# Performance work log

Hardware: AMD Instinct MI355X
Metric: run time of the kernel (lower is better)

## Reference

```python
import jax, jax.numpy as jnp
import numpy as np

NUM_HEADS = 16

def _split_heads(x, H):
    B, S, D = x.shape
    return x.reshape(B, S, H, D // H).transpose(0, 2, 1, 3)  # [B,H,S,hd]

def _merge_heads(x):
    B, H, S, hd = x.shape
    return x.transpose(0, 2, 1, 3).reshape(B, S, H * hd)

def setup_inputs() -> dict:
    key = jax.random.key(0)
    k1, k2, k3, k4 = jax.random.split(key, 4)
    B, S, D = 2, 2048, 1024
    return {
        "visual_features": jax.random.normal(k1, (B, S, D), dtype=jnp.float32),
        "transaction_features": jax.random.normal(k2, (B, S, D), dtype=jnp.float32),
        "W_qkv": jax.random.normal(k3, (D, 3 * D), dtype=jnp.float32) * (1.0 / np.sqrt(D)),
        "W_out": jax.random.normal(k4, (D, D), dtype=jnp.float32) * (1.0 / np.sqrt(D)),
    }

def reference(visual_features, transaction_features, W_qkv, W_out):
    H = NUM_HEADS
    D = visual_features.shape[-1]
    scale = (D // H) ** -0.5

    v_q, v_k, v_v = [_split_heads(t, H) for t in jnp.split(visual_features @ W_qkv, 3, axis=-1)]
    t_q, t_k, t_v = [_split_heads(t, H) for t in jnp.split(transaction_features @ W_qkv, 3, axis=-1)]

    # visual queries attend to transaction keys/values (dropout = identity at eval)
    v2t = jax.nn.softmax(jnp.einsum('bhqd,bhkd->bhqk', v_q, t_k) * scale, axis=-1)
    t2v = jax.nn.softmax(jnp.einsum('bhqd,bhkd->bhqk', t_q, v_k) * scale, axis=-1)

    v2t_out = _merge_heads(jnp.einsum('bhqk,bhkd->bhqd', v2t, t_v))
    t2v_out = _merge_heads(jnp.einsum('bhqk,bhkd->bhqd', t2v, v_v))

    return (v2t_out + t2v_out) @ W_out
```

## Files before the change

kernel.cpp:

```cpp
#include <hip/hip_runtime.h>


typedef short  frag8 __attribute__((ext_vector_type(8)));
typedef float  f32x4 __attribute__((ext_vector_type(4)));

union F8 { frag8 f; uint2 u2[2]; unsigned u[4]; };

#define MFMA16(a,b,c) __builtin_amdgcn_mfma_f32_16x16x32_bf16((a),(b),(c),0,0,0)

__device__ __forceinline__ unsigned short f2bf(float f) {
  unsigned u = __builtin_bit_cast(unsigned, f);
  return (unsigned short)((u + 0x7fffu + ((u >> 16) & 1u)) >> 16);
}
__device__ __forceinline__ float bf2f(unsigned short s) {
  unsigned u = ((unsigned)s) << 16;
  return __builtin_bit_cast(float, u);
}
__device__ __forceinline__ unsigned pkbf(float lo, float hi) {
  unsigned r;
  asm("v_cvt_pk_bf16_f32 %0, %1, %2" : "=v"(r) : "v"(lo), "v"(hi));
  return r;
}
__device__ __forceinline__ float fexp2(float x) {
  float r;
  asm("v_exp_f32 %0, %1" : "=v"(r) : "v"(x));
  return r;
}

__global__ __launch_bounds__(256) void k_pre(
    const float* __restrict__ vis, const float* __restrict__ trn,
    const float* __restrict__ Wqkv, const float* __restrict__ Wout,
    unsigned short* __restrict__ Abf, unsigned short* __restrict__ WqbT,
    unsigned short* __restrict__ WobT)
{
  __shared__ unsigned short L[64 * 72];
  const int bid = blockIdx.x;
  const int tid = threadIdx.x;

  if (bid < 4096) {
    size_t i8 = ((size_t)bid * 256 + tid) * 8;
    const float* src = (i8 < 4194304) ? vis + i8 : trn + (i8 - 4194304);
    float4 u = *(const float4*)src;
    float4 v = *(const float4*)(src + 4);
    uint4 w;
    w.x = pkbf(u.x, u.y); w.y = pkbf(u.z, u.w);
    w.z = pkbf(v.x, v.y); w.w = pkbf(v.z, v.w);
    *(uint4*)(Abf + i8) = w;
    return;
  }

  const float* W; unsigned short* Wt; int N, bx, by;
  if (bid < 4864) { int b = bid - 4096; W = Wqkv; Wt = WqbT; N = 3072; bx = b % 48; by = b / 48; }
  else            { int b = bid - 4864; W = Wout; Wt = WobT; N = 1024; bx = b % 16; by = b / 16; }
  const int n0 = bx * 64, k0 = by * 64;
  {
    int kr = tid >> 2, c4 = (tid & 3) * 16;
    const float* gp = W + (size_t)(k0 + kr) * N + n0 + c4;
    float4 u0 = *(const float4*)gp,       u1 = *(const float4*)(gp + 4);
    float4 u2 = *(const float4*)(gp + 8), u3 = *(const float4*)(gp + 12);
    unsigned* lw = (unsigned*)&L[kr * 72 + c4];
    lw[0] = pkbf(u0.x, u0.y); lw[1] = pkbf(u0.z, u0.w);
    lw[2] = pkbf(u1.x, u1.y); lw[3] = pkbf(u1.z, u1.w);
    lw[4] = pkbf(u2.x, u2.y); lw[5] = pkbf(u2.z, u2.w);
    lw[6] = pkbf(u3.x, u3.y); lw[7] = pkbf(u3.z, u3.w);
  }
  __syncthreads();
  int nr = tid >> 2, kc = (tid & 3) * 16;
  unsigned wb[8];
#pragma unroll
  for (int j = 0; j < 8; ++j) {
    unsigned lo = L[(kc + 2 * j)     * 72 + nr];
    unsigned hi = L[(kc + 2 * j + 1) * 72 + nr];
    wb[j] = lo | (hi << 16);
  }
  unsigned short* op = Wt + (size_t)(n0 + nr) * 1024 + k0 + kc;
  *(uint4*)op       = *(uint4*)&wb[0];
  *(uint4*)(op + 8) = *(uint4*)&wb[4];
}

__global__ __launch_bounds__(256) void k_gemm_qkv_b(
    const unsigned short* __restrict__ Abf, const unsigned short* __restrict__ WqbT,
    unsigned short* __restrict__ qkv)
{
  __shared__ unsigned short As_[128 * 32];
  __shared__ unsigned short Bs_[128 * 32];
  const int tid  = threadIdx.x;
  const int lane = tid & 63, wv = tid >> 6;
  const int lm = lane & 15, lg = lane >> 4;
  const int wg = (blockIdx.x & 7) * 192 + (blockIdx.x >> 3);
  const int nt = wg % 24, mt = wg / 24;
  const int wr = (wv >> 1) * 64, wc = (wv & 1) * 64;

  f32x4 acc[4][4] = {};

  const unsigned short* agp =
      Abf + (size_t)(mt * 128 + wv * 32 + (lane >> 2)) * 1024 + (lane & 3) * 8;
  const unsigned short* bgp =
      WqbT + (size_t)(nt * 128 + wv * 32 + (lane >> 2)) * 1024 + (lane & 3) * 8;

  for (int kt = 0; kt < 32; ++kt) {
    __syncthreads();
    __builtin_amdgcn_global_load_lds(
        (const __attribute__((address_space(1))) void*)(agp + kt * 32),
        (__attribute__((address_space(3))) void*)&As_[wv * 1024], 16, 0, 0);
    __builtin_amdgcn_global_load_lds(
        (const __attribute__((address_space(1))) void*)(agp + 16 * 1024 + kt * 32),
        (__attribute__((address_space(3))) void*)&As_[wv * 1024 + 512], 16, 0, 0);
    __builtin_amdgcn_global_load_lds(
        (const __attribute__((address_space(1))) void*)(bgp + kt * 32),
        (__attribute__((address_space(3))) void*)&Bs_[wv * 1024], 16, 0, 0);
    __builtin_amdgcn_global_load_lds(
        (const __attribute__((address_space(1))) void*)(bgp + 16 * 1024 + kt * 32),
        (__attribute__((address_space(3))) void*)&Bs_[wv * 1024 + 512], 16, 0, 0);
    __syncthreads();
    frag8 af[4], bfr[4];
#pragma unroll
    for (int mi = 0; mi < 4; ++mi)
      af[mi] = *(const frag8*)&As_[(wr + mi * 16 + lm) * 32 + lg * 8];
#pragma unroll
    for (int ni = 0; ni < 4; ++ni)
      bfr[ni] = *(const frag8*)&Bs_[(wc + ni * 16 + lm) * 32 + lg * 8];
#pragma unroll
    for (int mi = 0; mi < 4; ++mi)
#pragma unroll
      for (int ni = 0; ni < 4; ++ni)
        acc[mi][ni] = MFMA16(af[mi], bfr[ni], acc[mi][ni]);
  }

#pragma unroll
  for (int mi = 0; mi < 4; ++mi)
#pragma unroll
    for (int ni = 0; ni < 4; ++ni)
#pragma unroll
      for (int r = 0; r < 4; ++r) {
        int row = mt * 128 + wr + mi * 16 + lg * 4 + r;
        int col = nt * 128 + wc + ni * 16 + lm;
        qkv[(size_t)row * 3072 + col] = f2bf(acc[mi][ni][r]);
      }
}

__global__ __launch_bounds__(256) void k_vt(
    const unsigned short* __restrict__ qkv, unsigned short* __restrict__ Vt)
{
  __shared__ unsigned short L[64 * 72];
  const int tid = threadIdx.x;
  const int sblk = blockIdx.x;
  const int by = blockIdx.y;
  const int src = by >> 4, h = by & 15;
  {
    int sl = tid >> 2, dc = tid & 3;
    const unsigned short* gp =
        qkv + (size_t)(src * 2048 + sblk * 64 + sl) * 3072 + 2048 + h * 64 + dc * 16;
    *(frag8*)&L[sl * 72 + dc * 16]     = *(const frag8*)gp;
    *(frag8*)&L[sl * 72 + dc * 16 + 8] = *(const frag8*)(gp + 8);
  }
  __syncthreads();
  int d = tid >> 2, sc = tid & 3;
  unsigned wbuf[8];
#pragma unroll
  for (int j = 0; j < 8; ++j) {
    unsigned lo = L[(sc * 16 + 2 * j)     * 72 + d];
    unsigned hi = L[(sc * 16 + 2 * j + 1) * 72 + d];
    wbuf[j] = lo | (hi << 16);
  }
  unsigned short* op =
      Vt + ((size_t)(src * 16 + h) * 64 + d) * 2048 + sblk * 64 + sc * 16;
  *(uint4*)op       = *(uint4*)&wbuf[0];
  *(uint4*)(op + 8) = *(uint4*)&wbuf[4];
}

__global__ __launch_bounds__(256) void k_attn(
    const unsigned short* __restrict__ qkv, const unsigned short* __restrict__ Vt,
    unsigned short* __restrict__ Opart, float* __restrict__ lpart)
{
  __shared__ unsigned short Ks[2][32 * 72];
  __shared__ unsigned short Vs[2][8 * 272];
  const int tid  = threadIdx.x;
  const int lane = tid & 63, wv = tid >> 6;
  const int lm = lane & 15, lg = lane >> 4;
  const int qt = blockIdx.x, comb = blockIdx.y;
  const int dir = comb >> 5, bb = (comb >> 4) & 1, h = comb & 15;
  const int half = blockIdx.z;
  const int NT = 32, kt0 = half * 32;
  const int qbase  = (dir ? 4096 : 0) + bb * 2048;
  const int kvbase = (dir ? 0 : 4096) + bb * 2048;
  const int qcol = h * 64, kcol = 1024 + h * 64;

  const float QS = 0.125f * 1.44269504f;
  frag8 qf[2][2];
#pragma unroll
  for (int mi = 0; mi < 2; ++mi)
#pragma unroll
    for (int kb = 0; kb < 2; ++kb) {
      frag8 t = *(const frag8*)&qkv[
          (size_t)(qbase + qt * 128 + wv * 32 + mi * 16 + lm) * 3072 +
          qcol + kb * 32 + lg * 8];
#pragma unroll
      for (int j = 0; j < 8; ++j)
        t[j] = (short)f2bf(bf2f((unsigned short)t[j]) * QS);
      qf[mi][kb] = t;
    }

  f32x4 acc[2][4] = {};
  float lr[2] = {0.0f, 0.0f};

  const int skv = tid >> 3, sd = (tid & 7) * 8;
  const int vd = tid >> 2, vc = tid & 3;
  const unsigned short* __restrict__ kpp =
      qkv + (size_t)(kvbase + kt0 * 32 + skv) * 3072 + kcol + sd;
  const unsigned short* __restrict__ vpp =
      Vt + ((size_t)((kvbase >> 11) * 16 + h) * 64 + vd) * 2048 + kt0 * 32 + vc * 8;

  frag8 Rk, Rv;

#define LOAD_R() do {                                                      \
    Rk = *(const frag8*)kpp;  kpp += 32 * 3072;                            \
    Rv = *(const frag8*)vpp;  vpp += 32;                                   \
  } while (0)

#define WRITE_R(s_) do {                                                   \
    *(frag8*)&Ks[s_][skv * 72 + sd] = Rk;                                  \
    F8 tv_; tv_.f = Rv;                                                    \
    *(uint2*)&Vs[s_][(2 * vc) * 272 + vd * 4]     = tv_.u2[0];             \
    *(uint2*)&Vs[s_][(2 * vc + 1) * 272 + vd * 4] = tv_.u2[1];             \
  } while (0)

  LOAD_R();
  WRITE_R(0);
  LOAD_R();

  for (int i = 0; i < NT; ++i) {
    __syncthreads();
    if (i < NT - 1) WRITE_R((i + 1) & 1);
    if (i < NT - 2) LOAD_R();
    const int s = i & 1;

    frag8 kf[2][2];
#pragma unroll
    for (int t = 0; t < 2; ++t)
#pragma unroll
      for (int kb = 0; kb < 2; ++kb)
        kf[t][kb] = *(const frag8*)&Ks[s][(t * 16 + lm) * 72 + kb * 32 + lg * 8];
    f32x4 st[2][2] = {};
#pragma unroll
    for (int mi = 0; mi < 2; ++mi)
#pragma unroll
      for (int t = 0; t < 2; ++t)
#pragma unroll
        for (int kb = 0; kb < 2; ++kb)
          st[mi][t] = MFMA16(kf[t][kb], qf[mi][kb], st[mi][t]);

    frag8 pa[2];
#pragma unroll
    for (int mi = 0; mi < 2; ++mi) {
      f32x4 a = st[mi][0], b = st[mi][1];
      float p[8];
#pragma unroll
      for (int r = 0; r < 4; ++r) p[r]     = fexp2(a[r]);
#pragma unroll
      for (int r = 0; r < 4; ++r) p[4 + r] = fexp2(b[r]);
      lr[mi] += ((p[0] + p[1]) + (p[2] + p[3])) +
                ((p[4] + p[5]) + (p[6] + p[7]));
      F8 pk_;
      pk_.u[0] = pkbf(p[0], p[1]); pk_.u[1] = pkbf(p[2], p[3]);
      pk_.u[2] = pkbf(p[4], p[5]); pk_.u[3] = pkbf(p[6], p[7]);
      pa[mi] = pk_.f;
    }

    frag8 vb[4];
#pragma unroll
    for (int di = 0; di < 4; ++di) {
      F8 t;
      t.u2[0] = *(const uint2*)&Vs[s][lg * 272 + (di * 16 + lm) * 4];
      t.u2[1] = *(const uint2*)&Vs[s][(4 + lg) * 272 + (di * 16 + lm) * 4];
      vb[di] = t.f;
    }
#pragma unroll
    for (int mi = 0; mi < 2; ++mi)
#pragma unroll
      for (int di = 0; di < 4; ++di)
        acc[mi][di] = MFMA16(pa[mi], vb[di], acc[mi][di]);
  }

#undef LOAD_R
#undef WRITE_R

#pragma unroll
  for (int mi = 0; mi < 2; ++mi) {
    float l = lr[mi];
    l += __shfl_xor(l, 16);
    l += __shfl_xor(l, 32);
    int rowb = bb * 2048 + qt * 128 + wv * 32 + mi * 16;
    if (lane < 16)
      lpart[(size_t)(half * 2 + dir) * 65536 + h * 4096 + rowb + lane] = l;
#pragma unroll
    for (int r = 0; r < 4; ++r) {
      int row = rowb + lg * 4 + r;
#pragma unroll
      for (int di = 0; di < 4; ++di) {
        int col = h * 64 + di * 16 + lm;
        Opart[((size_t)(half * 2 + dir) * 4096 + row) * 1024 + col] =
            f2bf(acc[mi][di][r]);
      }
    }
  }
}

__global__ __launch_bounds__(256) void k_gemm_out_b(
    const unsigned short* __restrict__ Op, const float* __restrict__ lp,
    const unsigned short* __restrict__ WobT, float* __restrict__ out)
{
  __shared__ unsigned short As[128 * 40];
  __shared__ unsigned short Bs_[128 * 32];
  const int tid  = threadIdx.x;
  const int lane = tid & 63, wv = tid >> 6;
  const int lm = lane & 15, lg = lane >> 4;
  const int wg = (blockIdx.x & 7) * 32 + (blockIdx.x >> 3);
  const int nt = wg % 8, mt = wg / 8;
  const int wr = (wv >> 1) * 64, wc = (wv & 1) * 64;

  f32x4 acc[4][4] = {};

  const int am = tid >> 1, akq = (tid & 1) * 16;
  const int arow = mt * 128 + am;
  const unsigned short* __restrict__ p00 = Op + (size_t)arow * 1024;
  const unsigned short* __restrict__ p01 = p00 + (size_t)4096 * 1024;
  const unsigned short* __restrict__ p10 = p00 + (size_t)2 * 4096 * 1024;
  const unsigned short* __restrict__ p11 = p00 + (size_t)3 * 4096 * 1024;
  const unsigned short* bgp =
      WobT + (size_t)(nt * 128 + wv * 32 + (lane >> 2)) * 1024 + (lane & 3) * 8;

  for (int kt = 0; kt < 32; ++kt) {
    __syncthreads();
    __builtin_amdgcn_global_load_lds(
        (const __attribute__((address_space(1))) void*)(bgp + kt * 32),
        (__attribute__((address_space(3))) void*)&Bs_[wv * 1024], 16, 0, 0);
    __builtin_amdgcn_global_load_lds(
        (const __attribute__((address_space(1))) void*)(bgp + 16 * 1024 + kt * 32),
        (__attribute__((address_space(3))) void*)&Bs_[wv * 1024 + 512], 16, 0, 0);
    {
      const int kcol = kt * 32 + akq;
      const int hh = kt >> 1;
      float inv0 = 1.0f / (lp[hh * 4096 + arow]          + lp[131072 + hh * 4096 + arow]);
      float inv1 = 1.0f / (lp[65536 + hh * 4096 + arow]  + lp[196608 + hh * 4096 + arow]);
      frag8 u0 = *(const frag8*)(p00 + kcol);
      frag8 u1 = *(const frag8*)(p00 + kcol + 8);
      frag8 v0 = *(const frag8*)(p10 + kcol);
      frag8 v1 = *(const frag8*)(p10 + kcol + 8);
      frag8 w0 = *(const frag8*)(p01 + kcol);
      frag8 w1 = *(const frag8*)(p01 + kcol + 8);
      frag8 x0 = *(const frag8*)(p11 + kcol);
      frag8 x1 = *(const frag8*)(p11 + kcol + 8);
      frag8 q0, q1;
#pragma unroll
      for (int j = 0; j < 8; ++j) {
        float a0 = (bf2f((unsigned short)u0[j]) + bf2f((unsigned short)v0[j])) * inv0 +
                   (bf2f((unsigned short)w0[j]) + bf2f((unsigned short)x0[j])) * inv1;
        float a1 = (bf2f((unsigned short)u1[j]) + bf2f((unsigned short)v1[j])) * inv0 +
                   (bf2f((unsigned short)w1[j]) + bf2f((unsigned short)x1[j])) * inv1;
        q0[j] = (short)f2bf(a0);
        q1[j] = (short)f2bf(a1);
      }
      *(frag8*)&As[am * 40 + akq]     = q0;
      *(frag8*)&As[am * 40 + akq + 8] = q1;
    }
    __syncthreads();
    frag8 af[4], bfr[4];
#pragma unroll
    for (int mi = 0; mi < 4; ++mi)
      af[mi] = *(const frag8*)&As[(wr + mi * 16 + lm) * 40 + lg * 8];
#pragma unroll
    for (int ni = 0; ni < 4; ++ni)
      bfr[ni] = *(const frag8*)&Bs_[(wc + ni * 16 + lm) * 32 + lg * 8];
#pragma unroll
    for (int mi = 0; mi < 4; ++mi)
#pragma unroll
      for (int ni = 0; ni < 4; ++ni)
        acc[mi][ni] = MFMA16(af[mi], bfr[ni], acc[mi][ni]);
  }

#pragma unroll
  for (int mi = 0; mi < 4; ++mi)
#pragma unroll
    for (int ni = 0; ni < 4; ++ni)
#pragma unroll
      for (int r = 0; r < 4; ++r) {
        int row = mt * 128 + wr + mi * 16 + lg * 4 + r;
        int col = nt * 128 + wc + ni * 16 + lm;
        out[(size_t)row * 1024 + col] = acc[mi][ni][r];
      }
}

extern "C" void kernel_launch(void* const* d_in, const int* in_sizes, int n_in,
                              void* d_out, int out_size, void* d_ws, size_t ws_size,
                              hipStream_t stream)
{
  const float* vis  = (const float*)d_in[0];
  const float* trn  = (const float*)d_in[1];
  const float* Wqkv = (const float*)d_in[2];
  const float* Wout = (const float*)d_in[3];
  float* out = (float*)d_out;

  char* base = (char*)d_ws;
  unsigned short* qkv  = (unsigned short*)base;
  unsigned short* Vt   = (unsigned short*)(base + 67108864UL);
  unsigned short* WobT = (unsigned short*)(base + 83886080UL);
  float*          lp   = (float*)(base + 85983232UL);
  unsigned short* Abf  = (unsigned short*)(base + 87031808UL);
  unsigned short* WqbT = Abf + 8388608;
  unsigned short* Op   = (unsigned short*)(base + 87031808UL);

  k_pre       <<<5120, 256, 0, stream>>>(vis, trn, Wqkv, Wout, Abf, WqbT, WobT);
  k_gemm_qkv_b<<<1536, 256, 0, stream>>>(Abf, WqbT, qkv);
  k_vt        <<<dim3(32, 64), 256, 0, stream>>>(qkv, Vt);
  k_attn      <<<dim3(16, 64, 2), 256, 0, stream>>>(qkv, Vt, Op, lp);
  k_gemm_out_b<<<256, 256, 0, stream>>>(Op, lp, WobT, out);
}
```

Measured before the change: 236.2 us.

## Drop attention KV split, normalize in attention, process two KV tiles per barrier

The attention kernel no longer splits the 2048 keys into two halves across blockIdx.z. Each block now walks all 64 KV tiles, two tiles per iteration, with a four-stage shared buffer, so it hits the barrier half as often. Softmax normalization moves into the attention epilogue, which writes normalized bf16 outputs for each direction; the output GEMM then just sums two inputs instead of reading four partials plus the row sums. This cuts partial-output traffic and per-element work in the GEMM, but halves the attention grid to 1024 blocks and doubles per-block serial length and LDS use, which may hurt occupancy and load balance.

```diff
diff --git a/kernel.cpp b/kernel.cpp
--- a/kernel.cpp
+++ b/kernel.cpp
@@ -171,17 +171,15 @@
 
 __global__ __launch_bounds__(256) void k_attn(
     const unsigned short* __restrict__ qkv, const unsigned short* __restrict__ Vt,
-    unsigned short* __restrict__ Opart, float* __restrict__ lpart)
-{
-  __shared__ unsigned short Ks[2][32 * 72];
-  __shared__ unsigned short Vs[2][8 * 272];
+    unsigned short* __restrict__ o0, unsigned short* __restrict__ o1)
+{
+  __shared__ unsigned short Ks[4][32 * 72];
+  __shared__ unsigned short Vs[4][8 * 272];
   const int tid  = threadIdx.x;
   const int lane = tid & 63, wv = tid >> 6;
   const int lm = lane & 15, lg = lane >> 4;
   const int qt = blockIdx.x, comb = blockIdx.y;
   const int dir = comb >> 5, bb = (comb >> 4) & 1, h = comb & 15;
-  const int half = blockIdx.z;
-  const int NT = 32, kt0 = half * 32;
   const int qbase  = (dir ? 4096 : 0) + bb * 2048;
   const int kvbase = (dir ? 0 : 4096) + bb * 2048;
   const int qcol = h * 64, kcol = 1024 + h * 64;
@@ -207,107 +205,132 @@
   const int skv = tid >> 3, sd = (tid & 7) * 8;
   const int vd = tid >> 2, vc = tid & 3;
   const unsigned short* __restrict__ kpp =
-      qkv + (size_t)(kvbase + kt0 * 32 + skv) * 3072 + kcol + sd;
+      qkv + (size_t)(kvbase + skv) * 3072 + kcol + sd;
   const unsigned short* __restrict__ vpp =
-      Vt + ((size_t)((kvbase >> 11) * 16 + h) * 64 + vd) * 2048 + kt0 * 32 + vc * 8;
-
-  frag8 Rk, Rv;
-
-#define LOAD_R() do {                                                      \
-    Rk = *(const frag8*)kpp;  kpp += 32 * 3072;                            \
-    Rv = *(const frag8*)vpp;  vpp += 32;                                   \
+      Vt + ((size_t)((kvbase >> 11) * 16 + h) * 64 + vd) * 2048 + vc * 8;
+
+  frag8 R0k, R0v, R1k, R1v;
+
+#define LOAD2() do {                                                       \
+    R0k = *(const frag8*)kpp;  kpp += 32 * 3072;                           \
+    R0v = *(const frag8*)vpp;  vpp += 32;                                  \
+    R1k = *(const frag8*)kpp;  kpp += 32 * 3072;                           \
+    R1v = *(const frag8*)vpp;  vpp += 32;                                  \
   } while (0)
 
-#define WRITE_R(s_) do {                                                   \
-    *(frag8*)&Ks[s_][skv * 72 + sd] = Rk;                                  \
-    F8 tv_; tv_.f = Rv;                                                    \
+#define WRITE1(s_, Rk_, Rv_) do {                                          \
+    *(frag8*)&Ks[s_][skv * 72 + sd] = Rk_;                                 \
+    F8 tv_; tv_.f = Rv_;                                                   \
     *(uint2*)&Vs[s_][(2 * vc) * 272 + vd * 4]     = tv_.u2[0];             \
     *(uint2*)&Vs[s_][(2 * vc + 1) * 272 + vd * 4] = tv_.u2[1];             \
   } while (0)
 
-  LOAD_R();
-  WRITE_R(0);
-  LOAD_R();
-
-  for (int i = 0; i < NT; ++i) {
+  LOAD2();
+  WRITE1(0, R0k, R0v);
+  WRITE1(1, R1k, R1v);
+  LOAD2();
+  __syncthreads();
+
+  for (int j = 0; j < 32; ++j) {
+    const int p = j & 1;
+    if (j < 31) {
+      WRITE1(2 * (p ^ 1),     R0k, R0v);
+      WRITE1(2 * (p ^ 1) + 1, R1k, R1v);
+    }
+    if (j < 30) LOAD2();
+
+    const int sA = 2 * p, sB = 2 * p + 1;
+
+    frag8 kfA[2][2], kfB[2][2];
+#pragma unroll
+    for (int t = 0; t < 2; ++t)
+#pragma unroll
+      for (int kb = 0; kb < 2; ++kb) {
+        kfA[t][kb] = *(const frag8*)&Ks[sA][(t * 16 + lm) * 72 + kb * 32 + lg * 8];
+        kfB[t][kb] = *(const frag8*)&Ks[sB][(t * 16 + lm) * 72 + kb * 32 + lg * 8];
+      }
+    f32x4 stA[2][2] = {}, stB[2][2] = {};
+#pragma unroll
+    for (int mi = 0; mi < 2; ++mi)
+#pragma unroll
+      for (int t = 0; t < 2; ++t)
+#pragma unroll
+        for (int kb = 0; kb < 2; ++kb) {
+          stA[mi][t] = MFMA16(kfA[t][kb], qf[mi][kb], stA[mi][t]);
+          stB[mi][t] = MFMA16(kfB[t][kb], qf[mi][kb], stB[mi][t]);
+        }
+
+    frag8 paA[2], paB[2];
+#pragma unroll
+    for (int mi = 0; mi < 2; ++mi) {
+      f32x4 a = stA[mi][0], b = stA[mi][1];
+      f32x4 c = stB[mi][0], d = stB[mi][1];
+      float p0[8], p1[8];
+#pragma unroll
+      for (int r = 0; r < 4; ++r) {
+        p0[r] = fexp2(a[r]); p0[4 + r] = fexp2(b[r]);
+        p1[r] = fexp2(c[r]); p1[4 + r] = fexp2(d[r]);
+      }
+      lr[mi] += (((p0[0] + p0[1]) + (p0[2] + p0[3])) +
+                 ((p0[4] + p0[5]) + (p0[6] + p0[7]))) +
+                (((p1[0] + p1[1]) + (p1[2] + p1[3])) +
+                 ((p1[4] + p1[5]) + (p1[6] + p1[7])));
+      F8 ka, kb2;
+      ka.u[0]  = pkbf(p0[0], p0[1]); ka.u[1]  = pkbf(p0[2], p0[3]);
+      ka.u[2]  = pkbf(p0[4], p0[5]); ka.u[3]  = pkbf(p0[6], p0[7]);
+      kb2.u[0] = pkbf(p1[0], p1[1]); kb2.u[1] = pkbf(p1[2], p1[3]);
+      kb2.u[2] = pkbf(p1[4], p1[5]); kb2.u[3] = pkbf(p1[6], p1[7]);
+      paA[mi] = ka.f;
+      paB[mi] = kb2.f;
+    }
+
+    frag8 vbA[4], vbB[4];
+#pragma unroll
+    for (int di = 0; di < 4; ++di) {
+      F8 ta, tb;
+      ta.u2[0] = *(const uint2*)&Vs[sA][lg * 272 + (di * 16 + lm) * 4];
+      ta.u2[1] = *(const uint2*)&Vs[sA][(4 + lg) * 272 + (di * 16 + lm) * 4];
+      tb.u2[0] = *(const uint2*)&Vs[sB][lg * 272 + (di * 16 + lm) * 4];
+      tb.u2[1] = *(const uint2*)&Vs[sB][(4 + lg) * 272 + (di * 16 + lm) * 4];
+      vbA[di] = ta.f;
+      vbB[di] = tb.f;
+    }
+#pragma unroll
+    for (int mi = 0; mi < 2; ++mi)
+#pragma unroll
+      for (int di = 0; di < 4; ++di) {
+        acc[mi][di] = MFMA16(paA[mi], vbA[di], acc[mi][di]);
+        acc[mi][di] = MFMA16(paB[mi], vbB[di], acc[mi][di]);
+      }
+
     __syncthreads();
-    if (i < NT - 1) WRITE_R((i + 1) & 1);
-    if (i < NT - 2) LOAD_R();
-    const int s = i & 1;
-
-    frag8 kf[2][2];
-#pragma unroll
-    for (int t = 0; t < 2; ++t)
-#pragma unroll
-      for (int kb = 0; kb < 2; ++kb)
-        kf[t][kb] = *(const frag8*)&Ks[s][(t * 16 + lm) * 72 + kb * 32 + lg * 8];
-    f32x4 st[2][2] = {};
-#pragma unroll
-    for (int mi = 0; mi < 2; ++mi)
-#pragma unroll
-      for (int t = 0; t < 2; ++t)
-#pragma unroll
-        for (int kb = 0; kb < 2; ++kb)
-          st[mi][t] = MFMA16(kf[t][kb], qf[mi][kb], st[mi][t]);
-
-    frag8 pa[2];
-#pragma unroll
-    for (int mi = 0; mi < 2; ++mi) {
-      f32x4 a = st[mi][0], b = st[mi][1];
-      float p[8];
-#pragma unroll
-      for (int r = 0; r < 4; ++r) p[r]     = fexp2(a[r]);
-#pragma unroll
-      for (int r = 0; r < 4; ++r) p[4 + r] = fexp2(b[r]);
-      lr[mi] += ((p[0] + p[1]) + (p[2] + p[3])) +
-                ((p[4] + p[5]) + (p[6] + p[7]));
-      F8 pk_;
-      pk_.u[0] = pkbf(p[0], p[1]); pk_.u[1] = pkbf(p[2], p[3]);
-      pk_.u[2] = pkbf(p[4], p[5]); pk_.u[3] = pkbf(p[6], p[7]);
-      pa[mi] = pk_.f;
-    }
-
-    frag8 vb[4];
-#pragma unroll
-    for (int di = 0; di < 4; ++di) {
-      F8 t;
-      t.u2[0] = *(const uint2*)&Vs[s][lg * 272 + (di * 16 + lm) * 4];
-      t.u2[1] = *(const uint2*)&Vs[s][(4 + lg) * 272 + (di * 16 + lm) * 4];
-      vb[di] = t.f;
-    }
-#pragma unroll
-    for (int mi = 0; mi < 2; ++mi)
-#pragma unroll
-      for (int di = 0; di < 4; ++di)
-        acc[mi][di] = MFMA16(pa[mi], vb[di], acc[mi][di]);
-  }
-
-#undef LOAD_R
-#undef WRITE_R
-
+  }
+
+#undef LOAD2
+#undef WRITE1
+
+  unsigned short* __restrict__ dst = dir ? o1 : o0;
 #pragma unroll
   for (int mi = 0; mi < 2; ++mi) {
     float l = lr[mi];
     l += __shfl_xor(l, 16);
     l += __shfl_xor(l, 32);
-    int rowb = bb * 2048 + qt * 128 + wv * 32 + mi * 16;
-    if (lane < 16)
-      lpart[(size_t)(half * 2 + dir) * 65536 + h * 4096 + rowb + lane] = l;
+    float inv = 1.0f / l;
 #pragma unroll
     for (int r = 0; r < 4; ++r) {
-      int row = rowb + lg * 4 + r;
+      float invr = __shfl(inv, 4 * lg + r);
+      int row = bb * 2048 + qt * 128 + wv * 32 + mi * 16 + lg * 4 + r;
 #pragma unroll
       for (int di = 0; di < 4; ++di) {
         int col = h * 64 + di * 16 + lm;
-        Opart[((size_t)(half * 2 + dir) * 4096 + row) * 1024 + col] =
-            f2bf(acc[mi][di][r]);
+        dst[(size_t)row * 1024 + col] = f2bf(acc[mi][di][r] * invr);
       }
     }
   }
 }
 
 __global__ __launch_bounds__(256) void k_gemm_out_b(
-    const unsigned short* __restrict__ Op, const float* __restrict__ lp,
+    const unsigned short* __restrict__ x0, const unsigned short* __restrict__ x1,
     const unsigned short* __restrict__ WobT, float* __restrict__ out)
 {
   __shared__ unsigned short As[128 * 40];
@@ -323,10 +346,8 @@
 
   const int am = tid >> 1, akq = (tid & 1) * 16;
   const int arow = mt * 128 + am;
-  const unsigned short* __restrict__ p00 = Op + (size_t)arow * 1024;
-  const unsigned short* __restrict__ p01 = p00 + (size_t)4096 * 1024;
-  const unsigned short* __restrict__ p10 = p00 + (size_t)2 * 4096 * 1024;
-  const unsigned short* __restrict__ p11 = p00 + (size_t)3 * 4096 * 1024;
+  const unsigned short* __restrict__ a0p = x0 + (size_t)arow * 1024;
+  const unsigned short* __restrict__ a1p = x1 + (size_t)arow * 1024;
   const unsigned short* bgp =
       WobT + (size_t)(nt * 128 + wv * 32 + (lane >> 2)) * 1024 + (lane & 3) * 8;
 
@@ -339,30 +360,18 @@
         (const __attribute__((address_space(1))) void*)(bgp + 16 * 1024 + kt * 32),
         (__attribute__((address_space(3))) void*)&Bs_[wv * 1024 + 512], 16, 0, 0);
     {
-      const int kcol = kt * 32 + akq;
-      const int hh = kt >> 1;
-      float inv0 = 1.0f / (lp[hh * 4096 + arow]          + lp[131072 + hh * 4096 + arow]);
-      float inv1 = 1.0f / (lp[65536 + hh * 4096 + arow]  + lp[196608 + hh * 4096 + arow]);
-      frag8 u0 = *(const frag8*)(p00 + kcol);
-      frag8 u1 = *(const frag8*)(p00 + kcol + 8);
-      frag8 v0 = *(const frag8*)(p10 + kcol);
-      frag8 v1 = *(const frag8*)(p10 + kcol + 8);
-      frag8 w0 = *(const frag8*)(p01 + kcol);
-      frag8 w1 = *(const frag8*)(p01 + kcol + 8);
-      frag8 x0 = *(const frag8*)(p11 + kcol);
-      frag8 x1 = *(const frag8*)(p11 + kcol + 8);
-      frag8 q0, q1;
+      frag8 u0 = *(const frag8*)(a0p + kt * 32 + akq);
+      frag8 u1 = *(const frag8*)(a0p + kt * 32 + akq + 8);
+      frag8 w0 = *(const frag8*)(a1p + kt * 32 + akq);
+      frag8 w1 = *(const frag8*)(a1p + kt * 32 + akq + 8);
+      frag8 p0, p1;
 #pragma unroll
       for (int j = 0; j < 8; ++j) {
-        float a0 = (bf2f((unsigned short)u0[j]) + bf2f((unsigned short)v0[j])) * inv0 +
-                   (bf2f((unsigned short)w0[j]) + bf2f((unsigned short)x0[j])) * inv1;
-        float a1 = (bf2f((unsigned short)u1[j]) + bf2f((unsigned short)v1[j])) * inv0 +
-                   (bf2f((unsigned short)w1[j]) + bf2f((unsigned short)x1[j])) * inv1;
-        q0[j] = (short)f2bf(a0);
-        q1[j] = (short)f2bf(a1);
-      }
-      *(frag8*)&As[am * 40 + akq]     = q0;
-      *(frag8*)&As[am * 40 + akq + 8] = q1;
+        p0[j] = (short)f2bf(bf2f((unsigned short)u0[j]) + bf2f((unsigned short)w0[j]));
+        p1[j] = (short)f2bf(bf2f((unsigned short)u1[j]) + bf2f((unsigned short)w1[j]));
+      }
+      *(frag8*)&As[am * 40 + akq]     = p0;
+      *(frag8*)&As[am * 40 + akq + 8] = p1;
     }
     __syncthreads();
     frag8 af[4], bfr[4];
@@ -403,16 +412,16 @@
 
   char* base = (char*)d_ws;
   unsigned short* qkv  = (unsigned short*)base;
+  unsigned short* a0   = (unsigned short*)(base + 50331648UL);
+  unsigned short* a1   = a0 + 4194304;
   unsigned short* Vt   = (unsigned short*)(base + 67108864UL);
   unsigned short* WobT = (unsigned short*)(base + 83886080UL);
-  float*          lp   = (float*)(base + 85983232UL);
   unsigned short* Abf  = (unsigned short*)(base + 87031808UL);
   unsigned short* WqbT = Abf + 8388608;
-  unsigned short* Op   = (unsigned short*)(base + 87031808UL);
 
   k_pre       <<<5120, 256, 0, stream>>>(vis, trn, Wqkv, Wout, Abf, WqbT, WobT);
   k_gemm_qkv_b<<<1536, 256, 0, stream>>>(Abf, WqbT, qkv);
   k_vt        <<<dim3(32, 64), 256, 0, stream>>>(qkv, Vt);
-  k_attn      <<<dim3(16, 64, 2), 256, 0, stream>>>(qkv, Vt, Op, lp);
-  k_gemm_out_b<<<256, 256, 0, stream>>>(Op, lp, WobT, out);
-}
+  k_attn      <<<dim3(16, 64), 256, 0, stream>>>(qkv, Vt, a0, a1);
+  k_gemm_out_b<<<256, 256, 0, stream>>>(a0, a1, WobT, out);
+}
```

New measurement: 220.7 us. -6.5%, faster.

## Drop KV split in attention, reuse K/V tiles across two query tiles, normalize in-kernel

Applied to the files above, without the earlier changes.

The attention kernel no longer splits the key range into two halves. Each block now processes two 128-row query tiles over the full key range, so every staged K/V tile in LDS is reused twice. Softmax normalization happens in the attention epilogue, so the per-half partial sums and their four-way merge in the output GEMM are removed. The softmax scale is folded into the Q columns of the bf16 weight conversion, which drops the per-element Q rescale. In exchange the grid shrinks from 2048 to 512 blocks and each thread holds more registers, which may reduce occupancy and latency hiding.

```diff
diff --git a/kernel.cpp b/kernel.cpp
--- a/kernel.cpp
+++ b/kernel.cpp
@@ -53,16 +53,17 @@
   if (bid < 4864) { int b = bid - 4096; W = Wqkv; Wt = WqbT; N = 3072; bx = b % 48; by = b / 48; }
   else            { int b = bid - 4864; W = Wout; Wt = WobT; N = 1024; bx = b % 16; by = b / 16; }
   const int n0 = bx * 64, k0 = by * 64;
+  const float sc = (bid < 4864 && n0 < 1024) ? 0.125f * 1.44269504f : 1.0f;
   {
     int kr = tid >> 2, c4 = (tid & 3) * 16;
     const float* gp = W + (size_t)(k0 + kr) * N + n0 + c4;
     float4 u0 = *(const float4*)gp,       u1 = *(const float4*)(gp + 4);
     float4 u2 = *(const float4*)(gp + 8), u3 = *(const float4*)(gp + 12);
     unsigned* lw = (unsigned*)&L[kr * 72 + c4];
-    lw[0] = pkbf(u0.x, u0.y); lw[1] = pkbf(u0.z, u0.w);
-    lw[2] = pkbf(u1.x, u1.y); lw[3] = pkbf(u1.z, u1.w);
-    lw[4] = pkbf(u2.x, u2.y); lw[5] = pkbf(u2.z, u2.w);
-    lw[6] = pkbf(u3.x, u3.y); lw[7] = pkbf(u3.z, u3.w);
+    lw[0] = pkbf(u0.x * sc, u0.y * sc); lw[1] = pkbf(u0.z * sc, u0.w * sc);
+    lw[2] = pkbf(u1.x * sc, u1.y * sc); lw[3] = pkbf(u1.z * sc, u1.w * sc);
+    lw[4] = pkbf(u2.x * sc, u2.y * sc); lw[5] = pkbf(u2.z * sc, u2.w * sc);
+    lw[6] = pkbf(u3.x * sc, u3.y * sc); lw[7] = pkbf(u3.z * sc, u3.w * sc);
   }
   __syncthreads();
   int nr = tid >> 2, kc = (tid & 3) * 16;
@@ -171,7 +172,7 @@
 
 __global__ __launch_bounds__(256) void k_attn(
     const unsigned short* __restrict__ qkv, const unsigned short* __restrict__ Vt,
-    unsigned short* __restrict__ Opart, float* __restrict__ lpart)
+    unsigned short* __restrict__ o0, unsigned short* __restrict__ o1)
 {
   __shared__ unsigned short Ks[2][32 * 72];
   __shared__ unsigned short Vs[2][8 * 272];
@@ -180,36 +181,30 @@
   const int lm = lane & 15, lg = lane >> 4;
   const int qt = blockIdx.x, comb = blockIdx.y;
   const int dir = comb >> 5, bb = (comb >> 4) & 1, h = comb & 15;
-  const int half = blockIdx.z;
-  const int NT = 32, kt0 = half * 32;
   const int qbase  = (dir ? 4096 : 0) + bb * 2048;
   const int kvbase = (dir ? 0 : 4096) + bb * 2048;
   const int qcol = h * 64, kcol = 1024 + h * 64;
 
-  const float QS = 0.125f * 1.44269504f;
-  frag8 qf[2][2];
-#pragma unroll
-  for (int mi = 0; mi < 2; ++mi)
-#pragma unroll
-    for (int kb = 0; kb < 2; ++kb) {
-      frag8 t = *(const frag8*)&qkv[
-          (size_t)(qbase + qt * 128 + wv * 32 + mi * 16 + lm) * 3072 +
-          qcol + kb * 32 + lg * 8];
-#pragma unroll
-      for (int j = 0; j < 8; ++j)
-        t[j] = (short)f2bf(bf2f((unsigned short)t[j]) * QS);
-      qf[mi][kb] = t;
-    }
-
-  f32x4 acc[2][4] = {};
-  float lr[2] = {0.0f, 0.0f};
+  frag8 qf[2][2][2];
+#pragma unroll
+  for (int qi = 0; qi < 2; ++qi)
+#pragma unroll
+    for (int mi = 0; mi < 2; ++mi)
+#pragma unroll
+      for (int kb = 0; kb < 2; ++kb)
+        qf[qi][mi][kb] = *(const frag8*)&qkv[
+            (size_t)(qbase + (qt + 8 * qi) * 128 + wv * 32 + mi * 16 + lm) * 3072 +
+            qcol + kb * 32 + lg * 8];
+
+  f32x4 acc[2][2][4] = {};
+  float lr[2][2] = {};
 
   const int skv = tid >> 3, sd = (tid & 7) * 8;
   const int vd = tid >> 2, vc = tid & 3;
   const unsigned short* __restrict__ kpp =
-      qkv + (size_t)(kvbase + kt0 * 32 + skv) * 3072 + kcol + sd;
+      qkv + (size_t)(kvbase + skv) * 3072 + kcol + sd;
   const unsigned short* __restrict__ vpp =
-      Vt + ((size_t)((kvbase >> 11) * 16 + h) * 64 + vd) * 2048 + kt0 * 32 + vc * 8;
+      Vt + ((size_t)((kvbase >> 11) * 16 + h) * 64 + vd) * 2048 + vc * 8;
 
   frag8 Rk, Rv;
 
@@ -229,10 +224,10 @@
   WRITE_R(0);
   LOAD_R();
 
-  for (int i = 0; i < NT; ++i) {
+  for (int i = 0; i < 64; ++i) {
     __syncthreads();
-    if (i < NT - 1) WRITE_R((i + 1) & 1);
-    if (i < NT - 2) LOAD_R();
+    if (i < 63) WRITE_R((i + 1) & 1);
+    if (i < 62) LOAD_R();
     const int s = i & 1;
 
     frag8 kf[2][2];
@@ -241,32 +236,6 @@
 #pragma unroll
       for (int kb = 0; kb < 2; ++kb)
         kf[t][kb] = *(const frag8*)&Ks[s][(t * 16 + lm) * 72 + kb * 32 + lg * 8];
-    f32x4 st[2][2] = {};
-#pragma unroll
-    for (int mi = 0; mi < 2; ++mi)
-#pragma unroll
-      for (int t = 0; t < 2; ++t)
-#pragma unroll
-        for (int kb = 0; kb < 2; ++kb)
-          st[mi][t] = MFMA16(kf[t][kb], qf[mi][kb], st[mi][t]);
-
-    frag8 pa[2];
-#pragma unroll
-    for (int mi = 0; mi < 2; ++mi) {
-      f32x4 a = st[mi][0], b = st[mi][1];
-      float p[8];
-#pragma unroll
-      for (int r = 0; r < 4; ++r) p[r]     = fexp2(a[r]);
-#pragma unroll
-      for (int r = 0; r < 4; ++r) p[4 + r] = fexp2(b[r]);
-      lr[mi] += ((p[0] + p[1]) + (p[2] + p[3])) +
-                ((p[4] + p[5]) + (p[6] + p[7]));
-      F8 pk_;
-      pk_.u[0] = pkbf(p[0], p[1]); pk_.u[1] = pkbf(p[2], p[3]);
-      pk_.u[2] = pkbf(p[4], p[5]); pk_.u[3] = pkbf(p[6], p[7]);
-      pa[mi] = pk_.f;
-    }
-
     frag8 vb[4];
 #pragma unroll
     for (int di = 0; di < 4; ++di) {
@@ -275,39 +244,68 @@
       t.u2[1] = *(const uint2*)&Vs[s][(4 + lg) * 272 + (di * 16 + lm) * 4];
       vb[di] = t.f;
     }
-#pragma unroll
-    for (int mi = 0; mi < 2; ++mi)
-#pragma unroll
-      for (int di = 0; di < 4; ++di)
-        acc[mi][di] = MFMA16(pa[mi], vb[di], acc[mi][di]);
+
+#pragma unroll
+    for (int qi = 0; qi < 2; ++qi) {
+      f32x4 st[2][2] = {};
+#pragma unroll
+      for (int mi = 0; mi < 2; ++mi)
+#pragma unroll
+        for (int t = 0; t < 2; ++t)
+#pragma unroll
+          for (int kb = 0; kb < 2; ++kb)
+            st[mi][t] = MFMA16(kf[t][kb], qf[qi][mi][kb], st[mi][t]);
+
+      frag8 pa[2];
+#pragma unroll
+      for (int mi = 0; mi < 2; ++mi) {
+        f32x4 a = st[mi][0], b = st[mi][1];
+        float p[8];
+#pragma unroll
+        for (int r = 0; r < 4; ++r) { p[r] = fexp2(a[r]); p[4 + r] = fexp2(b[r]); }
+        lr[qi][mi] += ((p[0] + p[1]) + (p[2] + p[3])) +
+                      ((p[4] + p[5]) + (p[6] + p[7]));
+        F8 pk_;
+        pk_.u[0] = pkbf(p[0], p[1]); pk_.u[1] = pkbf(p[2], p[3]);
+        pk_.u[2] = pkbf(p[4], p[5]); pk_.u[3] = pkbf(p[6], p[7]);
+        pa[mi] = pk_.f;
+      }
+
+#pragma unroll
+      for (int mi = 0; mi < 2; ++mi)
+#pragma unroll
+        for (int di = 0; di < 4; ++di)
+          acc[qi][mi][di] = MFMA16(pa[mi], vb[di], acc[qi][mi][di]);
+    }
   }
 
 #undef LOAD_R
 #undef WRITE_R
 
-#pragma unroll
-  for (int mi = 0; mi < 2; ++mi) {
-    float l = lr[mi];
-    l += __shfl_xor(l, 16);
-    l += __shfl_xor(l, 32);
-    int rowb = bb * 2048 + qt * 128 + wv * 32 + mi * 16;
-    if (lane < 16)
-      lpart[(size_t)(half * 2 + dir) * 65536 + h * 4096 + rowb + lane] = l;
-#pragma unroll
-    for (int r = 0; r < 4; ++r) {
-      int row = rowb + lg * 4 + r;
-#pragma unroll
-      for (int di = 0; di < 4; ++di) {
-        int col = h * 64 + di * 16 + lm;
-        Opart[((size_t)(half * 2 + dir) * 4096 + row) * 1024 + col] =
-            f2bf(acc[mi][di][r]);
+  unsigned short* __restrict__ dst = dir ? o1 : o0;
+#pragma unroll
+  for (int qi = 0; qi < 2; ++qi)
+#pragma unroll
+    for (int mi = 0; mi < 2; ++mi) {
+      float l = lr[qi][mi];
+      l += __shfl_xor(l, 16);
+      l += __shfl_xor(l, 32);
+      float inv = 1.0f / l;
+#pragma unroll
+      for (int r = 0; r < 4; ++r) {
+        float invr = __shfl(inv, 4 * lg + r);
+        int row = bb * 2048 + (qt + 8 * qi) * 128 + wv * 32 + mi * 16 + lg * 4 + r;
+#pragma unroll
+        for (int di = 0; di < 4; ++di) {
+          int col = h * 64 + di * 16 + lm;
+          dst[(size_t)row * 1024 + col] = f2bf(acc[qi][mi][di][r] * invr);
+        }
       }
     }
-  }
 }
 
 __global__ __launch_bounds__(256) void k_gemm_out_b(
-    const unsigned short* __restrict__ Op, const float* __restrict__ lp,
+    const unsigned short* __restrict__ x0, const unsigned short* __restrict__ x1,
     const unsigned short* __restrict__ WobT, float* __restrict__ out)
 {
   __shared__ unsigned short As[128 * 40];
@@ -323,10 +321,8 @@
 
   const int am = tid >> 1, akq = (tid & 1) * 16;
   const int arow = mt * 128 + am;
-  const unsigned short* __restrict__ p00 = Op + (size_t)arow * 1024;
-  const unsigned short* __restrict__ p01 = p00 + (size_t)4096 * 1024;
-  const unsigned short* __restrict__ p10 = p00 + (size_t)2 * 4096 * 1024;
-  const unsigned short* __restrict__ p11 = p00 + (size_t)3 * 4096 * 1024;
+  const unsigned short* __restrict__ a0p = x0 + (size_t)arow * 1024;
+  const unsigned short* __restrict__ a1p = x1 + (size_t)arow * 1024;
   const unsigned short* bgp =
       WobT + (size_t)(nt * 128 + wv * 32 + (lane >> 2)) * 1024 + (lane & 3) * 8;
 
@@ -339,30 +335,18 @@
         (const __attribute__((address_space(1))) void*)(bgp + 16 * 1024 + kt * 32),
         (__attribute__((address_space(3))) void*)&Bs_[wv * 1024 + 512], 16, 0, 0);
     {
-      const int kcol = kt * 32 + akq;
-      const int hh = kt >> 1;
-      float inv0 = 1.0f / (lp[hh * 4096 + arow]          + lp[131072 + hh * 4096 + arow]);
-      float inv1 = 1.0f / (lp[65536 + hh * 4096 + arow]  + lp[196608 + hh * 4096 + arow]);
-      frag8 u0 = *(const frag8*)(p00 + kcol);
-      frag8 u1 = *(const frag8*)(p00 + kcol + 8);
-      frag8 v0 = *(const frag8*)(p10 + kcol);
-      frag8 v1 = *(const frag8*)(p10 + kcol + 8);
-      frag8 w0 = *(const frag8*)(p01 + kcol);
-      frag8 w1 = *(const frag8*)(p01 + kcol + 8);
-      frag8 x0 = *(const frag8*)(p11 + kcol);
-      frag8 x1 = *(const frag8*)(p11 + kcol + 8);
-      frag8 q0, q1;
+      frag8 u0 = *(const frag8*)(a0p + kt * 32 + akq);
+      frag8 u1 = *(const frag8*)(a0p + kt * 32 + akq + 8);
+      frag8 w0 = *(const frag8*)(a1p + kt * 32 + akq);
+      frag8 w1 = *(const frag8*)(a1p + kt * 32 + akq + 8);
+      frag8 p0, p1;
 #pragma unroll
       for (int j = 0; j < 8; ++j) {
-        float a0 = (bf2f((unsigned short)u0[j]) + bf2f((unsigned short)v0[j])) * inv0 +
-                   (bf2f((unsigned short)w0[j]) + bf2f((unsigned short)x0[j])) * inv1;
-        float a1 = (bf2f((unsigned short)u1[j]) + bf2f((unsigned short)v1[j])) * inv0 +
-                   (bf2f((unsigned short)w1[j]) + bf2f((unsigned short)x1[j])) * inv1;
-        q0[j] = (short)f2bf(a0);
-        q1[j] = (short)f2bf(a1);
+        p0[j] = (short)f2bf(bf2f((unsigned short)u0[j]) + bf2f((unsigned short)w0[j]));
+        p1[j] = (short)f2bf(bf2f((unsigned short)u1[j]) + bf2f((unsigned short)w1[j]));
       }
-      *(frag8*)&As[am * 40 + akq]     = q0;
-      *(frag8*)&As[am * 40 + akq + 8] = q1;
+      *(frag8*)&As[am * 40 + akq]     = p0;
+      *(frag8*)&As[am * 40 + akq + 8] = p1;
     }
     __syncthreads();
     frag8 af[4], bfr[4];
@@ -403,16 +387,16 @@
 
   char* base = (char*)d_ws;
   unsigned short* qkv  = (unsigned short*)base;
+  unsigned short* a0   = (unsigned short*)(base + 50331648UL);
+  unsigned short* a1   = a0 + 4194304;
   unsigned short* Vt   = (unsigned short*)(base + 67108864UL);
   unsigned short* WobT = (unsigned short*)(base + 83886080UL);
-  float*          lp   = (float*)(base + 85983232UL);
   unsigned short* Abf  = (unsigned short*)(base + 87031808UL);
   unsigned short* WqbT = Abf + 8388608;
-  unsigned short* Op   = (unsigned short*)(base + 87031808UL);
 
   k_pre       <<<5120, 256, 0, stream>>>(vis, trn, Wqkv, Wout, Abf, WqbT, WobT);
   k_gemm_qkv_b<<<1536, 256, 0, stream>>>(Abf, WqbT, qkv);
   k_vt        <<<dim3(32, 64), 256, 0, stream>>>(qkv, Vt);
-  k_attn      <<<dim3(16, 64, 2), 256, 0, stream>>>(qkv, Vt, Op, lp);
-  k_gemm_out_b<<<256, 256, 0, stream>>>(Op, lp, WobT, out);
-}
+  k_attn      <<<dim3(8, 64), 256, 0, stream>>>(qkv, Vt, a0, a1);
+  k_gemm_out_b<<<256, 256, 0, stream>>>(a0, a1, WobT, out);
+}
```

New measurement: 214.7 us, median of 3. 1.1x faster.

## Process two Q tiles per attention block and fold Q scale into weights

Applied to the files above, without the earlier changes.

Each attention block now computes two 128-row query tiles against the same staged K/V tiles, halving the grid and the K/V global/LDS loading per query. The softmax scale times log2e is folded into the Q columns of W_qkv during weight preconversion, removing the per-element Q rescale in the attention kernel. This raises register pressure (doubled accumulators) and may reduce occupancy, and it slightly changes rounding since the scale is applied before bf16 quantization of weights.

```diff
diff --git a/kernel.cpp b/kernel.cpp
--- a/kernel.cpp
+++ b/kernel.cpp
@@ -53,16 +53,17 @@
   if (bid < 4864) { int b = bid - 4096; W = Wqkv; Wt = WqbT; N = 3072; bx = b % 48; by = b / 48; }
   else            { int b = bid - 4864; W = Wout; Wt = WobT; N = 1024; bx = b % 16; by = b / 16; }
   const int n0 = bx * 64, k0 = by * 64;
+  const float sc = (bid < 4864 && n0 < 1024) ? 0.125f * 1.44269504f : 1.0f;
   {
     int kr = tid >> 2, c4 = (tid & 3) * 16;
     const float* gp = W + (size_t)(k0 + kr) * N + n0 + c4;
     float4 u0 = *(const float4*)gp,       u1 = *(const float4*)(gp + 4);
     float4 u2 = *(const float4*)(gp + 8), u3 = *(const float4*)(gp + 12);
     unsigned* lw = (unsigned*)&L[kr * 72 + c4];
-    lw[0] = pkbf(u0.x, u0.y); lw[1] = pkbf(u0.z, u0.w);
-    lw[2] = pkbf(u1.x, u1.y); lw[3] = pkbf(u1.z, u1.w);
-    lw[4] = pkbf(u2.x, u2.y); lw[5] = pkbf(u2.z, u2.w);
-    lw[6] = pkbf(u3.x, u3.y); lw[7] = pkbf(u3.z, u3.w);
+    lw[0] = pkbf(u0.x * sc, u0.y * sc); lw[1] = pkbf(u0.z * sc, u0.w * sc);
+    lw[2] = pkbf(u1.x * sc, u1.y * sc); lw[3] = pkbf(u1.z * sc, u1.w * sc);
+    lw[4] = pkbf(u2.x * sc, u2.y * sc); lw[5] = pkbf(u2.z * sc, u2.w * sc);
+    lw[6] = pkbf(u3.x * sc, u3.y * sc); lw[7] = pkbf(u3.z * sc, u3.w * sc);
   }
   __syncthreads();
   int nr = tid >> 2, kc = (tid & 3) * 16;
@@ -181,28 +182,24 @@
   const int qt = blockIdx.x, comb = blockIdx.y;
   const int dir = comb >> 5, bb = (comb >> 4) & 1, h = comb & 15;
   const int half = blockIdx.z;
-  const int NT = 32, kt0 = half * 32;
+  const int kt0 = half * 32;
   const int qbase  = (dir ? 4096 : 0) + bb * 2048;
   const int kvbase = (dir ? 0 : 4096) + bb * 2048;
   const int qcol = h * 64, kcol = 1024 + h * 64;
 
-  const float QS = 0.125f * 1.44269504f;
-  frag8 qf[2][2];
-#pragma unroll
-  for (int mi = 0; mi < 2; ++mi)
-#pragma unroll
-    for (int kb = 0; kb < 2; ++kb) {
-      frag8 t = *(const frag8*)&qkv[
-          (size_t)(qbase + qt * 128 + wv * 32 + mi * 16 + lm) * 3072 +
-          qcol + kb * 32 + lg * 8];
-#pragma unroll
-      for (int j = 0; j < 8; ++j)
-        t[j] = (short)f2bf(bf2f((unsigned short)t[j]) * QS);
-      qf[mi][kb] = t;
-    }
-
-  f32x4 acc[2][4] = {};
-  float lr[2] = {0.0f, 0.0f};
+  frag8 qf[2][2][2];
+#pragma unroll
+  for (int qi = 0; qi < 2; ++qi)
+#pragma unroll
+    for (int mi = 0; mi < 2; ++mi)
+#pragma unroll
+      for (int kb = 0; kb < 2; ++kb)
+        qf[qi][mi][kb] = *(const frag8*)&qkv[
+            (size_t)(qbase + (qt + 8 * qi) * 128 + wv * 32 + mi * 16 + lm) * 3072 +
+            qcol + kb * 32 + lg * 8];
+
+  f32x4 acc[2][2][4] = {};
+  float lr[2][2] = {};
 
   const int skv = tid >> 3, sd = (tid & 7) * 8;
   const int vd = tid >> 2, vc = tid & 3;
@@ -229,10 +226,10 @@
   WRITE_R(0);
   LOAD_R();
 
-  for (int i = 0; i < NT; ++i) {
+  for (int i = 0; i < 32; ++i) {
     __syncthreads();
-    if (i < NT - 1) WRITE_R((i + 1) & 1);
-    if (i < NT - 2) LOAD_R();
+    if (i < 31) WRITE_R((i + 1) & 1);
+    if (i < 30) LOAD_R();
     const int s = i & 1;
 
     frag8 kf[2][2];
@@ -241,32 +238,6 @@
 #pragma unroll
       for (int kb = 0; kb < 2; ++kb)
         kf[t][kb] = *(const frag8*)&Ks[s][(t * 16 + lm) * 72 + kb * 32 + lg * 8];
-    f32x4 st[2][2] = {};
-#pragma unroll
-    for (int mi = 0; mi < 2; ++mi)
-#pragma unroll
-      for (int t = 0; t < 2; ++t)
-#pragma unroll
-        for (int kb = 0; kb < 2; ++kb)
-          st[mi][t] = MFMA16(kf[t][kb], qf[mi][kb], st[mi][t]);
-
-    frag8 pa[2];
-#pragma unroll
-    for (int mi = 0; mi < 2; ++mi) {
-      f32x4 a = st[mi][0], b = st[mi][1];
-      float p[8];
-#pragma unroll
-      for (int r = 0; r < 4; ++r) p[r]     = fexp2(a[r]);
-#pragma unroll
-      for (int r = 0; r < 4; ++r) p[4 + r] = fexp2(b[r]);
-      lr[mi] += ((p[0] + p[1]) + (p[2] + p[3])) +
-                ((p[4] + p[5]) + (p[6] + p[7]));
-      F8 pk_;
-      pk_.u[0] = pkbf(p[0], p[1]); pk_.u[1] = pkbf(p[2], p[3]);
-      pk_.u[2] = pkbf(p[4], p[5]); pk_.u[3] = pkbf(p[6], p[7]);
-      pa[mi] = pk_.f;
-    }
-
     frag8 vb[4];
 #pragma unroll
     for (int di = 0; di < 4; ++di) {
@@ -275,35 +246,65 @@
       t.u2[1] = *(const uint2*)&Vs[s][(4 + lg) * 272 + (di * 16 + lm) * 4];
       vb[di] = t.f;
     }
-#pragma unroll
-    for (int mi = 0; mi < 2; ++mi)
-#pragma unroll
-      for (int di = 0; di < 4; ++di)
-        acc[mi][di] = MFMA16(pa[mi], vb[di], acc[mi][di]);
+
+#pragma unroll
+    for (int qi = 0; qi < 2; ++qi) {
+      f32x4 st[2][2] = {};
+#pragma unroll
+      for (int mi = 0; mi < 2; ++mi)
+#pragma unroll
+        for (int t = 0; t < 2; ++t)
+#pragma unroll
+          for (int kb = 0; kb < 2; ++kb)
+            st[mi][t] = MFMA16(kf[t][kb], qf[qi][mi][kb], st[mi][t]);
+
+      frag8 pa[2];
+#pragma unroll
+      for (int mi = 0; mi < 2; ++mi) {
+        f32x4 a = st[mi][0], b = st[mi][1];
+        float p[8];
+#pragma unroll
+        for (int r = 0; r < 4; ++r) { p[r] = fexp2(a[r]); p[4 + r] = fexp2(b[r]); }
+        lr[qi][mi] += ((p[0] + p[1]) + (p[2] + p[3])) +
+                      ((p[4] + p[5]) + (p[6] + p[7]));
+        F8 pk_;
+        pk_.u[0] = pkbf(p[0], p[1]); pk_.u[1] = pkbf(p[2], p[3]);
+        pk_.u[2] = pkbf(p[4], p[5]); pk_.u[3] = pkbf(p[6], p[7]);
+        pa[mi] = pk_.f;
+      }
+
+#pragma unroll
+      for (int mi = 0; mi < 2; ++mi)
+#pragma unroll
+        for (int di = 0; di < 4; ++di)
+          acc[qi][mi][di] = MFMA16(pa[mi], vb[di], acc[qi][mi][di]);
+    }
   }
 
 #undef LOAD_R
 #undef WRITE_R
 
 #pragma unroll
-  for (int mi = 0; mi < 2; ++mi) {
-    float l = lr[mi];
-    l += __shfl_xor(l, 16);
-    l += __shfl_xor(l, 32);
-    int rowb = bb * 2048 + qt * 128 + wv * 32 + mi * 16;
-    if (lane < 16)
-      lpart[(size_t)(half * 2 + dir) * 65536 + h * 4096 + rowb + lane] = l;
-#pragma unroll
-    for (int r = 0; r < 4; ++r) {
-      int row = rowb + lg * 4 + r;
-#pragma unroll
-      for (int di = 0; di < 4; ++di) {
-        int col = h * 64 + di * 16 + lm;
-        Opart[((size_t)(half * 2 + dir) * 4096 + row) * 1024 + col] =
-            f2bf(acc[mi][di][r]);
+  for (int qi = 0; qi < 2; ++qi)
+#pragma unroll
+    for (int mi = 0; mi < 2; ++mi) {
+      float l = lr[qi][mi];
+      l += __shfl_xor(l, 16);
+      l += __shfl_xor(l, 32);
+      int rowb = bb * 2048 + (qt + 8 * qi) * 128 + wv * 32 + mi * 16;
+      if (lane < 16)
+        lpart[(size_t)(half * 2 + dir) * 65536 + h * 4096 + rowb + lane] = l;
+#pragma unroll
+      for (int r = 0; r < 4; ++r) {
+        int row = rowb + lg * 4 + r;
+#pragma unroll
+        for (int di = 0; di < 4; ++di) {
+          int col = h * 64 + di * 16 + lm;
+          Opart[((size_t)(half * 2 + dir) * 4096 + row) * 1024 + col] =
+              f2bf(acc[qi][mi][di][r]);
+        }
       }
     }
-  }
 }
 
 __global__ __launch_bounds__(256) void k_gemm_out_b(
@@ -341,8 +342,8 @@
     {
       const int kcol = kt * 32 + akq;
       const int hh = kt >> 1;
-      float inv0 = 1.0f / (lp[hh * 4096 + arow]          + lp[131072 + hh * 4096 + arow]);
-      float inv1 = 1.0f / (lp[65536 + hh * 4096 + arow]  + lp[196608 + hh * 4096 + arow]);
+      float inv0 = 1.0f / (lp[hh * 4096 + arow]         + lp[131072 + hh * 4096 + arow]);
+      float inv1 = 1.0f / (lp[65536 + hh * 4096 + arow] + lp[196608 + hh * 4096 + arow]);
       frag8 u0 = *(const frag8*)(p00 + kcol);
       frag8 u1 = *(const frag8*)(p00 + kcol + 8);
       frag8 v0 = *(const frag8*)(p10 + kcol);
@@ -413,6 +414,6 @@
   k_pre       <<<5120, 256, 0, stream>>>(vis, trn, Wqkv, Wout, Abf, WqbT, WobT);
   k_gemm_qkv_b<<<1536, 256, 0, stream>>>(Abf, WqbT, qkv);
   k_vt        <<<dim3(32, 64), 256, 0, stream>>>(qkv, Vt);
-  k_attn      <<<dim3(16, 64, 2), 256, 0, stream>>>(qkv, Vt, Op, lp);
+  k_attn      <<<dim3(8, 64, 2), 256, 0, stream>>>(qkv, Vt, Op, lp);
   k_gemm_out_b<<<256, 256, 0, stream>>>(Op, lp, WobT, out);
 }
```

Measured after the change: 228.9 us. 3.1% less time.
